# Kernel optimization log

Hardware: AMD Instinct MI355X
Metric: run time of the kernel (lower is better)

Reference implementation:

```python
import jax, jax.numpy as jnp
import numpy as np

N = 100000        # nodes
E = 1600000       # edges (avg degree 16)
IN = 128          # in_channels
HID = 256         # hidden_channels
OUT = 2           # out_channels
G = 512           # num graphs in batch


def setup_inputs() -> dict:
    key = jax.random.key(0)
    ks = jax.random.split(key, 10)
    x = jax.random.normal(ks[0], (N, IN), dtype=jnp.float32)
    edge_index = jax.random.randint(ks[1], (2, E), 0, N, dtype=jnp.int64)
    # sorted graph assignment, every graph non-empty (PyG-style batching)
    batch = (jnp.arange(N, dtype=jnp.int64) * G) // N
    s = 1.0 / np.sqrt(IN)
    sh = 1.0 / np.sqrt(2 * HID)
    sh1 = 1.0 / np.sqrt(HID)
    W_l = jax.random.uniform(ks[2], (HID, IN), jnp.float32, -s, s)   # SAGE lin_l (neighbors)
    b_l = jax.random.uniform(ks[3], (HID,), jnp.float32, -s, s)
    W_r = jax.random.uniform(ks[4], (HID, IN), jnp.float32, -s, s)   # SAGE lin_r (root), no bias
    W0 = jax.random.uniform(ks[5], (HID, IN), jnp.float32, -s, s)    # lin0
    b0 = jax.random.uniform(ks[5], (HID,), jnp.float32, -s, s)
    W1 = jax.random.uniform(ks[6], (HID, 2 * HID), jnp.float32, -sh, sh)  # lin1
    b1 = jax.random.uniform(ks[7], (HID,), jnp.float32, -sh, sh)
    W2 = jax.random.uniform(ks[8], (OUT, HID), jnp.float32, -sh1, sh1)    # lin2
    b2 = jax.random.uniform(ks[9], (OUT,), jnp.float32, -sh1, sh1)
    return {"x": x, "edge_index": edge_index, "batch": batch,
            "W_l": W_l, "b_l": b_l, "W_r": W_r,
            "W0": W0, "b0": b0, "W1": W1, "b1": b1, "W2": W2, "b2": b2}


def reference(x, edge_index, batch, W_l, b_l, W_r, W0, b0, W1, b1, W2, b2):
    src, dst = edge_index[0], edge_index[1]
    # SAGEConv: mean-aggregate neighbor features (gather -> scatter-add -> normalize)
    msg_sum = jax.ops.segment_sum(x[src], dst, num_segments=N)          # [N, IN]
    deg = jax.ops.segment_sum(jnp.ones((E,), x.dtype), dst, num_segments=N)
    aggr = msg_sum / jnp.maximum(deg, 1.0)[:, None]
    h = jax.nn.relu(aggr @ W_l.T + b_l + x @ W_r.T)                     # [N, HID]
    # global max pool per graph
    hp = jax.ops.segment_max(h, batch, num_segments=G)                  # [G, HID]
    # root node = first node of each graph (batch is sorted)
    root = jnp.searchsorted(batch, jnp.arange(G, dtype=batch.dtype))    # [G]
    news = jax.nn.relu(x[root] @ W0.T + b0)                             # [G, HID]
    h = jax.nn.relu(jnp.concatenate([news, hp], axis=-1) @ W1.T + b1)   # [G, HID]
    h = h @ W2.T + b2                                                   # [G, OUT]
    return jax.nn.log_softmax(h, axis=-1)
```

## Files before the change

### kernel.cpp

```cpp
#include <hip/hip_runtime.h>
#include <hip/hip_bf16.h>
#include <math.h>
#include <stdint.h>

#define IN_C 128
#define HID  256
#define OUT_C 2

#define BSHIFT 8
#define BNODES 256
#define EPB 4096
#define HISTB 784
#define PADB 768

typedef __attribute__((ext_vector_type(8))) short short8;
typedef __attribute__((ext_vector_type(4))) float f32x4;
typedef __attribute__((ext_vector_type(2))) float f32x2;

#if defined(__has_builtin)
#if __has_builtin(__builtin_amdgcn_cvt_pk_f32_fp8) && __has_builtin(__builtin_amdgcn_cvt_pk_fp8_f32)
#define HAVE_FP8_CVT 1
#endif
#endif

__device__ __forceinline__ ushort f2bf(float f) {
  uint32_t u = __float_as_uint(f);
  uint32_t r = u + 0x7FFF + ((u >> 16) & 1);
  return (ushort)(r >> 16);
}
__device__ __forceinline__ float bf2f(ushort b) {
  return __uint_as_float(((uint32_t)b) << 16);
}

#ifndef HAVE_FP8_CVT
__device__ __forceinline__ uint32_t f2fp8_1(float f) {
  uint32_t u = __float_as_uint(f);
  uint32_t s = (u >> 24) & 0x80;
  float a = fabsf(f);
  if (a >= 448.f) return s | 0x7E;
  if (a < 0.015625f) {
    uint32_t m = (uint32_t)(a * 512.f + 0.5f);
    return s | m;
  }
  uint32_t r = u & 0x7fffffff;
  r += 0x7FFFF + ((r >> 20) & 1);
  uint32_t e = (r >> 23) - 127;
  if ((int)e > 8) return s | 0x7E;
  return s | ((e + 7) << 3) | ((r >> 20) & 7);
}
__device__ __forceinline__ float fp8_2f(uint32_t b) {
  uint32_t s = (b & 0x80) << 24;
  uint32_t e = (b >> 3) & 0xF, m = b & 7;
  if (e == 0) { float f = (float)m * 0.001953125f; return s ? -f : f; }
  return __uint_as_float(s | ((e + 120) << 23) | (m << 20));
}
#endif

__device__ __forceinline__ void acc8f8v(f32x2* s, uint2 v) {
#ifdef HAVE_FP8_CVT
  s[0] += __builtin_amdgcn_cvt_pk_f32_fp8(v.x, false);
  s[1] += __builtin_amdgcn_cvt_pk_f32_fp8(v.x, true);
  s[2] += __builtin_amdgcn_cvt_pk_f32_fp8(v.y, false);
  s[3] += __builtin_amdgcn_cvt_pk_f32_fp8(v.y, true);
#else
  s[0].x += fp8_2f(v.x & 0xff);         s[0].y += fp8_2f((v.x >> 8) & 0xff);
  s[1].x += fp8_2f((v.x >> 16) & 0xff); s[1].y += fp8_2f(v.x >> 24);
  s[2].x += fp8_2f(v.y & 0xff);         s[2].y += fp8_2f((v.y >> 8) & 0xff);
  s[3].x += fp8_2f((v.y >> 16) & 0xff); s[3].y += fp8_2f(v.y >> 24);
#endif
}


__global__ void k_prep(const float* __restrict__ x, ushort* __restrict__ xb,
                       uint32_t* __restrict__ xf8, int n4,
                       const float* __restrict__ Wl, const float* __restrict__ Wr,
                       ushort* __restrict__ Wcat,
                       const float* __restrict__ W0, ushort* __restrict__ W0b,
                       const float* __restrict__ W1, ushort* __restrict__ W1b,
                       const int* __restrict__ batch, int* __restrict__ root, int n,
                       const int* __restrict__ dst, int E, int* __restrict__ bcount,
                       float* __restrict__ hp, int hp4) {
  __shared__ int h[512];
  int t = threadIdx.x;
  int i = blockIdx.x * 256 + t;
  if (i < n4) {
    float4 v = ((const float4*)x)[i];
    ushort4 o = {f2bf(v.x), f2bf(v.y), f2bf(v.z), f2bf(v.w)};
    ((ushort4*)xb)[i] = o;
#ifdef HAVE_FP8_CVT
    int p = __builtin_amdgcn_cvt_pk_fp8_f32(v.x, v.y, 0, false);
    p = __builtin_amdgcn_cvt_pk_fp8_f32(v.z, v.w, p, true);
    xf8[i] = (uint32_t)p;
#else
    xf8[i] = f2fp8_1(v.x) | (f2fp8_1(v.y) << 8) | (f2fp8_1(v.z) << 16) |
             (f2fp8_1(v.w) << 24);
#endif
  }
  if (i < 32) xf8[(size_t)n * 32 + i] = 0;
  if (i < HID * (2 * IN_C) / 4) {
    int c = i >> 6, c4 = (i & 63) * 4;
    float4 v = (c4 < IN_C) ? *(const float4*)(Wl + (size_t)c * IN_C + c4)
                           : *(const float4*)(Wr + (size_t)c * IN_C + (c4 - IN_C));
    ushort4 o = {f2bf(v.x), f2bf(v.y), f2bf(v.z), f2bf(v.w)};
    *(ushort4*)(Wcat + (size_t)c * (2 * IN_C) + c4) = o;
  }
  if (i < HID * IN_C / 4) {
    float4 v = ((const float4*)W0)[i];
    ushort4 o = {f2bf(v.x), f2bf(v.y), f2bf(v.z), f2bf(v.w)};
    ((ushort4*)W0b)[i] = o;
  }
  if (i < HID * 2 * HID / 4) {
    float4 v = ((const float4*)W1)[i];
    ushort4 o = {f2bf(v.x), f2bf(v.y), f2bf(v.z), f2bf(v.w)};
    ((ushort4*)W1b)[i] = o;
  }
  if (i < hp4) ((float4*)hp)[i] = make_float4(0.f, 0.f, 0.f, 0.f);
  if (i < n) {
    int g = batch[i];
    if (i == 0 || batch[i - 1] != g) root[g] = i;
  }
  if (blockIdx.x < HISTB) {
    h[t] = 0; h[t + 256] = 0;
    __syncthreads();
    int E4 = E >> 2;
    const int4* d4 = (const int4*)dst;
    for (int e = blockIdx.x * 256 + t; e < E4; e += HISTB * 256) {
      int4 d = d4[e];
      atomicAdd(&h[d.x >> BSHIFT], 1);
      atomicAdd(&h[d.y >> BSHIFT], 1);
      atomicAdd(&h[d.z >> BSHIFT], 1);
      atomicAdd(&h[d.w >> BSHIFT], 1);
    }
    if (blockIdx.x == 0)
      for (int e = (E4 << 2) + t; e < E; e += 256)
        atomicAdd(&h[dst[e] >> BSHIFT], 1);
    __syncthreads();
    if (h[t]) atomicAdd(&bcount[t], h[t]);
    if (h[t + 256]) atomicAdd(&bcount[t + 256], h[t + 256]);
  }
}


__global__ __launch_bounds__(256) void k_scatter(
    const int* __restrict__ src, const int* __restrict__ dst,
    const int* __restrict__ bcount, int* __restrict__ cursor0,
    uint32_t* __restrict__ rec, int E) {
  __shared__ int sBB[512];
  __shared__ int stmp[256];
  __shared__ int h[512];
  __shared__ int hb[512];
  __shared__ int lcur[512];
  int t = threadIdx.x;
  int c0 = bcount[2 * t], c1 = bcount[2 * t + 1];
  stmp[t] = c0 + c1;
  h[2 * t] = 0; h[2 * t + 1] = 0;
  lcur[2 * t] = 0; lcur[2 * t + 1] = 0;
  __syncthreads();
  for (int off = 1; off < 256; off <<= 1) {
    int v = (t >= off) ? stmp[t - off] : 0;
    __syncthreads();
    stmp[t] += v;
    __syncthreads();
  }
  int ex = stmp[t] - (c0 + c1);
  sBB[2 * t] = ex;
  sBB[2 * t + 1] = ex + c0;
  __syncthreads();

  int e0 = blockIdx.x * EPB;
  int e1 = e0 + EPB < E ? e0 + EPB : E;
  int cnt = e1 - e0;
  int cnt4 = cnt >> 2;
  const int4* d4 = (const int4*)(dst + e0);
  const int4* s4 = (const int4*)(src + e0);

  for (int i = t; i < cnt4; i += 256) {
    int4 d = d4[i];
    atomicAdd(&h[d.x >> BSHIFT], 1);
    atomicAdd(&h[d.y >> BSHIFT], 1);
    atomicAdd(&h[d.z >> BSHIFT], 1);
    atomicAdd(&h[d.w >> BSHIFT], 1);
  }
  for (int i = (cnt4 << 2) + t; i < cnt; i += 256)
    atomicAdd(&h[dst[e0 + i] >> BSHIFT], 1);
  __syncthreads();
  for (int j = t; j < 512; j += 256)
    if (h[j]) hb[j] = sBB[j] + atomicAdd(&cursor0[j], h[j]);
  __syncthreads();
  for (int i = t; i < cnt4; i += 256) {
    int4 d = d4[i];
    int4 s = s4[i];
    {
      int b = d.x >> BSHIFT; int r = atomicAdd(&lcur[b], 1);
      rec[hb[b] + r] = ((uint32_t)s.x << BSHIFT) | ((uint32_t)d.x & (BNODES - 1));
    }
    {
      int b = d.y >> BSHIFT; int r = atomicAdd(&lcur[b], 1);
      rec[hb[b] + r] = ((uint32_t)s.y << BSHIFT) | ((uint32_t)d.y & (BNODES - 1));
    }
    {
      int b = d.z >> BSHIFT; int r = atomicAdd(&lcur[b], 1);
      rec[hb[b] + r] = ((uint32_t)s.z << BSHIFT) | ((uint32_t)d.z & (BNODES - 1));
    }
    {
      int b = d.w >> BSHIFT; int r = atomicAdd(&lcur[b], 1);
      rec[hb[b] + r] = ((uint32_t)s.w << BSHIFT) | ((uint32_t)d.w & (BNODES - 1));
    }
  }
  for (int i = (cnt4 << 2) + t; i < cnt; i += 256) {
    int d = dst[e0 + i];
    int b = d >> BSHIFT;
    int r = atomicAdd(&lcur[b], 1);
    rec[hb[b] + r] = ((uint32_t)src[e0 + i] << BSHIFT) | ((uint32_t)d & (BNODES - 1));
  }
}


__global__ __launch_bounds__(256) void k_csr(
    const uint32_t* __restrict__ rec, const int* __restrict__ bcount,
    int* __restrict__ row_start, int* __restrict__ deg,
    int* __restrict__ csr, int n, int zrow) {
  __shared__ int stmp[256];
  __shared__ int lexcl[256];
  __shared__ int ldeg[256];
  __shared__ int lcur[256];
  int t = threadIdx.x, b = blockIdx.x;
  int i2 = 2 * t;
  int v = ((i2 < b) ? bcount[i2] : 0) + ((i2 + 1 < b) ? bcount[i2 + 1] : 0);
  stmp[t] = v;
  ldeg[t] = 0;
  __syncthreads();
  for (int off = 128; off > 0; off >>= 1) {
    if (t < off) stmp[t] += stmp[t + off];
    __syncthreads();
  }
  int ebase = stmp[0];
  int ecnt = bcount[b];
  int padbase = ((ebase + 3) & ~3) + PADB * b;
  int node0 = b << BSHIFT;
  __syncthreads();

  const uint32_t* rb = rec + ebase;
  int ec4 = ecnt >> 2;
  for (int i = t; i < ec4; i += 256) {
    uint4 r = *(const uint4*)(rb + i * 4);
    atomicAdd(&ldeg[r.x & (BNODES - 1)], 1);
    atomicAdd(&ldeg[r.y & (BNODES - 1)], 1);
    atomicAdd(&ldeg[r.z & (BNODES - 1)], 1);
    atomicAdd(&ldeg[r.w & (BNODES - 1)], 1);
  }
  for (int i = (ec4 << 2) + t; i < ecnt; i += 256)
    atomicAdd(&ldeg[rb[i] & (BNODES - 1)], 1);
  __syncthreads();
  int d = ldeg[t];
  int P = (d + 3) & ~3;
  stmp[t] = P;
  __syncthreads();
  for (int off = 1; off < 256; off <<= 1) {
    int vv = (t >= off) ? stmp[t - off] : 0;
    __syncthreads();
    stmp[t] += vv;
    __syncthreads();
  }
  int excl = stmp[t] - P;
  lexcl[t] = excl;
  int rs = padbase + excl;
  int node = node0 + t;
  if (node < n) { row_start[node] = rs; deg[node] = d; }
  lcur[t] = 0;
  __syncthreads();
  for (int i = t; i < ec4; i += 256) {
    uint4 r = *(const uint4*)(rb + i * 4);
    {
      int li = r.x & (BNODES - 1); int k = atomicAdd(&lcur[li], 1);
      csr[padbase + lexcl[li] + k] = (int)(r.x >> BSHIFT);
    }
    {
      int li = r.y & (BNODES - 1); int k = atomicAdd(&lcur[li], 1);
      csr[padbase + lexcl[li] + k] = (int)(r.y >> BSHIFT);
    }
    {
      int li = r.z & (BNODES - 1); int k = atomicAdd(&lcur[li], 1);
      csr[padbase + lexcl[li] + k] = (int)(r.z >> BSHIFT);
    }
    {
      int li = r.w & (BNODES - 1); int k = atomicAdd(&lcur[li], 1);
      csr[padbase + lexcl[li] + k] = (int)(r.w >> BSHIFT);
    }
  }
  for (int i = (ec4 << 2) + t; i < ecnt; i += 256) {
    uint32_t r = rb[i];
    int li = r & (BNODES - 1);
    int k = atomicAdd(&lcur[li], 1);
    csr[padbase + lexcl[li] + k] = (int)(r >> BSHIFT);
  }
  for (int k = d; k < P; ++k) csr[rs + k] = zrow;
}


__global__ void k_aggr(const uint32_t* __restrict__ xf8, const int* __restrict__ csr,
                       const int* __restrict__ row_start, const int* __restrict__ deg,
                       ushort* __restrict__ aggr, int n) {
  int wid = threadIdx.x >> 6;
  int lane = threadIdx.x & 63;
  int q = lane >> 4, li = lane & 15;
  int node = blockIdx.x * 16 + wid * 4 + q;
  bool alive = node < n;
  int base = alive ? row_start[node] : 0;
  int d = alive ? deg[node] : 0;
  int P = (d + 3) & ~3;
  const uint2* xp = (const uint2*)xf8 + li;
  f32x2 s[4] = {};
  for (int i = 0; i < P; i += 4) {
    int4 ns = *(const int4*)(csr + base + i);
    uint2 a = xp[(size_t)ns.x * 16];
    uint2 b = xp[(size_t)ns.y * 16];
    uint2 c = xp[(size_t)ns.z * 16];
    uint2 e = xp[(size_t)ns.w * 16];
    acc8f8v(s, a); acc8f8v(s, b); acc8f8v(s, c); acc8f8v(s, e);
  }
  if (alive) {
    float inv = 1.0f / (float)(d > 1 ? d : 1);
    uint4 o;
    o.x = (uint32_t)f2bf(s[0].x * inv) | ((uint32_t)f2bf(s[0].y * inv) << 16);
    o.y = (uint32_t)f2bf(s[1].x * inv) | ((uint32_t)f2bf(s[1].y * inv) << 16);
    o.z = (uint32_t)f2bf(s[2].x * inv) | ((uint32_t)f2bf(s[2].y * inv) << 16);
    o.w = (uint32_t)f2bf(s[3].x * inv) | ((uint32_t)f2bf(s[3].y * inv) << 16);
    ((uint4*)(aggr + (size_t)node * IN_C))[li] = o;
  }
}


__global__ __launch_bounds__(256) void k_gemm_pool(
    const ushort* __restrict__ aggrb, const ushort* __restrict__ xb,
    const ushort* __restrict__ Wcat, const float* __restrict__ bl,
    const int* __restrict__ batch, float* __restrict__ hp, int n) {
  __shared__ float sbl[256];
  __shared__ int sBatch[64];

  int t = threadIdx.x;
  int n0 = blockIdx.x * 64;
  sbl[t] = bl[t];
  if (t < 64) sBatch[t] = (n0 + t < n) ? batch[n0 + t] : -1;
  __syncthreads();

  int lane = t & 63, w = t >> 6;
  int q = lane >> 4, m = lane & 15;

  const ushort* arow[4];
  const ushort* xrow[4];
  const ushort* wrow[4];
#pragma unroll
  for (int rt = 0; rt < 4; ++rt) {
    int gn = n0 + rt * 16 + m; gn = gn < n ? gn : n - 1;
    arow[rt] = aggrb + (size_t)gn * IN_C + q * 8;
    xrow[rt] = xb + (size_t)gn * IN_C + q * 8;
  }
#pragma unroll
  for (int ct = 0; ct < 4; ++ct)
    wrow[ct] = Wcat + (size_t)(w * 64 + ct * 16 + m) * (2 * IN_C) + q * 8;

  short8 afn[4], bfn[4];
#pragma unroll
  for (int rt = 0; rt < 4; ++rt) afn[rt] = *(const short8*)arow[rt];
#pragma unroll
  for (int ct = 0; ct < 4; ++ct) bfn[ct] = *(const short8*)wrow[ct];

  f32x4 acc[4][4] = {};
#pragma unroll
  for (int kc = 0; kc < 8; ++kc) {
    short8 af[4], bf[4];
#pragma unroll
    for (int rt = 0; rt < 4; ++rt) af[rt] = afn[rt];
#pragma unroll
    for (int ct = 0; ct < 4; ++ct) bf[ct] = bfn[ct];
    if (kc < 7) {
      int kn = kc + 1;
#pragma unroll
      for (int rt = 0; rt < 4; ++rt)
        afn[rt] = (kn < 4) ? *(const short8*)(arow[rt] + kn * 32)
                           : *(const short8*)(xrow[rt] + (kn - 4) * 32);
#pragma unroll
      for (int ct = 0; ct < 4; ++ct)
        bfn[ct] = *(const short8*)(wrow[ct] + kn * 32);
    }
#pragma unroll
    for (int rt = 0; rt < 4; ++rt)
#pragma unroll
      for (int ct = 0; ct < 4; ++ct)
        acc[rt][ct] = __builtin_amdgcn_mfma_f32_16x16x32_bf16(af[rt], bf[ct], acc[rt][ct], 0, 0, 0);
  }

  int last = n - 1 - n0; last = last < 63 ? last : 63;
  int gA = sBatch[0];
  int gB = sBatch[last];
#pragma unroll
  for (int ct = 0; ct < 4; ++ct) {
    int col = w * 64 + ct * 16 + m;
    float bias = sbl[col];
    float mA = 0.f, mB = 0.f;
#pragma unroll
    for (int rt = 0; rt < 4; ++rt) {
#pragma unroll
      for (int i = 0; i < 4; ++i) {
        int lr = rt * 16 + q * 4 + i;
        if (n0 + lr < n) {
          float v = fmaxf(acc[rt][ct][i] + bias, 0.f);
          if (sBatch[lr] == gA) mA = fmaxf(mA, v);
          else mB = fmaxf(mB, v);
        }
      }
    }
    mA = fmaxf(mA, __shfl_xor(mA, 16)); mA = fmaxf(mA, __shfl_xor(mA, 32));
    mB = fmaxf(mB, __shfl_xor(mB, 16)); mB = fmaxf(mB, __shfl_xor(mB, 32));
    if (q == 0) {
      atomicMax((int*)&hp[(size_t)gA * HID + col], __float_as_int(mA));
      if (gB != gA) atomicMax((int*)&hp[(size_t)gB * HID + col], __float_as_int(mB));
    }
  }
}


__global__ __launch_bounds__(256) void k_tail(
    const ushort* __restrict__ xb, const float* __restrict__ hp,
    const int* __restrict__ root,
    const ushort* __restrict__ W0b, const float* __restrict__ b0,
    const ushort* __restrict__ W1b, const float* __restrict__ b1,
    const float* __restrict__ W2, const float* __restrict__ b2,
    float* __restrict__ out, int G) {
  __shared__ ushort sCat[32][264];
  __shared__ int sRoot[32];
  __shared__ float pp[256][2];

  int t = threadIdx.x;
  int g0 = blockIdx.x * 32;
  if (t < 32) sRoot[t] = (g0 + t < G) ? root[g0 + t] : 0;
  __syncthreads();

  int lane = t & 63, w = t >> 6;
  int q = lane >> 4, m = lane & 15;

  const ushort* xrow[2];
#pragma unroll
  for (int rt = 0; rt < 2; ++rt)
    xrow[rt] = xb + (size_t)sRoot[rt * 16 + m] * IN_C;

  {
    f32x4 acc[2][4] = {};
#pragma unroll
    for (int kc = 0; kc < 4; ++kc) {
      short8 af[2], bf[4];
#pragma unroll
      for (int rt = 0; rt < 2; ++rt)
        af[rt] = *(const short8*)(xrow[rt] + kc * 32 + q * 8);
#pragma unroll
      for (int ct = 0; ct < 4; ++ct) {
        int col = w * 64 + ct * 16 + m;
        bf[ct] = *(const short8*)(W0b + (size_t)col * IN_C + kc * 32 + q * 8);
      }
#pragma unroll
      for (int rt = 0; rt < 2; ++rt)
#pragma unroll
        for (int ct = 0; ct < 4; ++ct)
          acc[rt][ct] = __builtin_amdgcn_mfma_f32_16x16x32_bf16(af[rt], bf[ct], acc[rt][ct], 0, 0, 0);
    }
#pragma unroll
    for (int ct = 0; ct < 4; ++ct) {
      int col = w * 64 + ct * 16 + m;
      float bias = b0[col];
#pragma unroll
      for (int rt = 0; rt < 2; ++rt)
#pragma unroll
        for (int i = 0; i < 4; ++i) {
          int row = rt * 16 + q * 4 + i;
          sCat[row][col] = f2bf(fmaxf(acc[rt][ct][i] + bias, 0.f));
        }
    }
  }
  __syncthreads();

  f32x4 acc2[2][4] = {};
  short8 bfn[4];
#pragma unroll
  for (int ct = 0; ct < 4; ++ct)
    bfn[ct] = *(const short8*)(W1b + (size_t)(w * 64 + ct * 16 + m) * (2 * HID) + q * 8);
#pragma unroll
  for (int kc = 0; kc < 8; ++kc) {
    short8 af[2], bf[4];
#pragma unroll
    for (int ct = 0; ct < 4; ++ct) bf[ct] = bfn[ct];
    if (kc < 7) {
#pragma unroll
      for (int ct = 0; ct < 4; ++ct)
        bfn[ct] = *(const short8*)(W1b + (size_t)(w * 64 + ct * 16 + m) * (2 * HID) +
                                   (kc + 1) * 32 + q * 8);
    }
#pragma unroll
    for (int rt = 0; rt < 2; ++rt)
      af[rt] = *(const short8*)&sCat[rt * 16 + m][kc * 32 + q * 8];
#pragma unroll
    for (int rt = 0; rt < 2; ++rt)
#pragma unroll
      for (int ct = 0; ct < 4; ++ct)
        acc2[rt][ct] = __builtin_amdgcn_mfma_f32_16x16x32_bf16(af[rt], bf[ct], acc2[rt][ct], 0, 0, 0);
  }
  __syncthreads();
#pragma unroll
  for (int it = 0; it < 8; ++it) {
    int idx = it * 256 + t;
    int r = idx >> 6, c4 = (idx & 63) * 4;
    if (g0 + r < G) {
      float4 v = *(const float4*)(hp + (size_t)(g0 + r) * HID + c4);
      ushort4 o = {f2bf(v.x), f2bf(v.y), f2bf(v.z), f2bf(v.w)};
      *(ushort4*)&sCat[r][c4] = o;
    }
  }
  __syncthreads();
#pragma unroll
  for (int ct = 0; ct < 4; ++ct)
    bfn[ct] = *(const short8*)(W1b + (size_t)(w * 64 + ct * 16 + m) * (2 * HID) + 8 * 32 + q * 8);
#pragma unroll
  for (int kc = 8; kc < 16; ++kc) {
    short8 af[2], bf[4];
#pragma unroll
    for (int ct = 0; ct < 4; ++ct) bf[ct] = bfn[ct];
    if (kc < 15) {
#pragma unroll
      for (int ct = 0; ct < 4; ++ct)
        bfn[ct] = *(const short8*)(W1b + (size_t)(w * 64 + ct * 16 + m) * (2 * HID) +
                                   (kc + 1) * 32 + q * 8);
    }
#pragma unroll
    for (int rt = 0; rt < 2; ++rt)
      af[rt] = *(const short8*)&sCat[rt * 16 + m][(kc - 8) * 32 + q * 8];
#pragma unroll
    for (int rt = 0; rt < 2; ++rt)
#pragma unroll
      for (int ct = 0; ct < 4; ++ct)
        acc2[rt][ct] = __builtin_amdgcn_mfma_f32_16x16x32_bf16(af[rt], bf[ct], acc2[rt][ct], 0, 0, 0);
  }
  __syncthreads();
#pragma unroll
  for (int ct = 0; ct < 4; ++ct) {
    int col = w * 64 + ct * 16 + m;
    float bias = b1[col];
#pragma unroll
    for (int rt = 0; rt < 2; ++rt)
#pragma unroll
      for (int i = 0; i < 4; ++i) {
        int row = rt * 16 + q * 4 + i;
        sCat[row][col] = f2bf(fmaxf(acc2[rt][ct][i] + bias, 0.f));
      }
  }
  __syncthreads();

  {
    int row = t >> 3, qq = t & 7;
    float p0 = 0.f, p1 = 0.f;
    for (int c = qq * 32; c < qq * 32 + 32; ++c) {
      float hv = bf2f(sCat[row][c]);
      p0 += hv * W2[c];
      p1 += hv * W2[HID + c];
    }
    pp[t][0] = p0; pp[t][1] = p1;
  }
  __syncthreads();
  if (t < 32 && g0 + t < G) {
    float l0 = b2[0], l1 = b2[1];
#pragma unroll
    for (int k = 0; k < 8; ++k) { l0 += pp[t * 8 + k][0]; l1 += pp[t * 8 + k][1]; }
    float mx = fmaxf(l0, l1);
    float ls = logf(expf(l0 - mx) + expf(l1 - mx));
    out[(size_t)(g0 + t) * 2 + 0] = l0 - mx - ls;
    out[(size_t)(g0 + t) * 2 + 1] = l1 - mx - ls;
  }
}


extern "C" void kernel_launch(void* const* d_in, const int* in_sizes, int n_in,
                              void* d_out, int out_size, void* d_ws, size_t ws_size,
                              hipStream_t stream) {
  const float* x  = (const float*)d_in[0];
  const int* ei   = (const int*)d_in[1];
  const int* batch= (const int*)d_in[2];
  const float* Wl = (const float*)d_in[3];
  const float* bl = (const float*)d_in[4];
  const float* Wr = (const float*)d_in[5];
  const float* W0 = (const float*)d_in[6];
  const float* b0 = (const float*)d_in[7];
  const float* W1 = (const float*)d_in[8];
  const float* b1 = (const float*)d_in[9];
  const float* W2 = (const float*)d_in[10];
  const float* b2 = (const float*)d_in[11];
  float* out = (float*)d_out;

  const int N = in_sizes[0] / IN_C;
  const int E = in_sizes[1] / 2;
  const int G = out_size / OUT_C;
  const int* src = ei;
  const int* dst = ei + E;
  const int NB = (N + BNODES - 1) >> BSHIFT;

  char* w = (char*)d_ws;
  int* deg       = (int*)w; w += (size_t)N * 4;
  int* row_start = (int*)w; w += (size_t)N * 4;
  int* bcount    = (int*)w; w += 2048;
  int* cursor0   = (int*)w; w += 2048;
  int* root      = (int*)w; w += (size_t)G * 4;
  w = (char*)(((uintptr_t)w + 255) & ~(uintptr_t)255);
  int* csr       = (int*)w; w += (size_t)(E + PADB * NB + 8192) * 4;
  w = (char*)(((uintptr_t)w + 255) & ~(uintptr_t)255);
  ushort* xb     = (ushort*)w; w += (size_t)N * IN_C * 2;
  uint32_t* xf8  = (uint32_t*)w; w += (size_t)(N + 1) * IN_C;
  ushort* aggrb  = (ushort*)w; w += (size_t)N * IN_C * 2;
  ushort* Wcat   = (ushort*)w; w += (size_t)HID * (2 * IN_C) * 2;
  ushort* W0b    = (ushort*)w; w += (size_t)HID * IN_C * 2;
  ushort* W1b    = (ushort*)w; w += (size_t)HID * 2 * HID * 2;
  float* hp      = (float*)w; w += (size_t)G * HID * 4;
  uint32_t* rec  = (uint32_t*)aggrb;

  hipMemsetAsync(bcount, 0, 4096, stream);

  int n4 = N * IN_C / 4;
  k_prep<<<(n4 + 255) / 256, 256, 0, stream>>>(
      x, xb, xf8, n4, Wl, Wr, Wcat, W0, W0b, W1, W1b, batch, root, N,
      dst, E, bcount, hp, G * HID / 4);
  k_scatter<<<(E + EPB - 1) / EPB, 256, 0, stream>>>(src, dst, bcount, cursor0, rec, E);
  k_csr<<<NB, 256, 0, stream>>>(rec, bcount, row_start, deg, csr, N, N);
  k_aggr<<<(N + 15) / 16, 256, 0, stream>>>(xf8, csr, row_start, deg, aggrb, N);
  k_gemm_pool<<<(N + 63) / 64, 256, 0, stream>>>(aggrb, xb, Wcat, bl, batch, hp, N);
  k_tail<<<(G + 31) / 32, 256, 0, stream>>>(xb, hp, root, W0b, b0, W1b, b1, W2, b2, out, G);
}
```

Before: 283.7 us.

## Fuse neighbor aggregation into GEMM+pool kernel via swizzled LDS tiles

New measurement: 275.4 us. 2.9% less time.

```diff
diff --git a/kernel.cpp b/kernel.cpp
--- a/kernel.cpp
+++ b/kernel.cpp
@@ -20,6 +20,9 @@
 #if defined(__has_builtin)
 #if __has_builtin(__builtin_amdgcn_cvt_pk_f32_fp8) && __has_builtin(__builtin_amdgcn_cvt_pk_fp8_f32)
 #define HAVE_FP8_CVT 1
+#endif
+#if __has_builtin(__builtin_amdgcn_global_load_lds)
+#define HAVE_GLL 1
 #endif
 #endif
 
@@ -298,91 +301,103 @@
 }
 
 
-__global__ void k_aggr(const uint32_t* __restrict__ xf8, const int* __restrict__ csr,
-                       const int* __restrict__ row_start, const int* __restrict__ deg,
-                       ushort* __restrict__ aggr, int n) {
-  int wid = threadIdx.x >> 6;
-  int lane = threadIdx.x & 63;
-  int q = lane >> 4, li = lane & 15;
-  int node = blockIdx.x * 16 + wid * 4 + q;
-  bool alive = node < n;
-  int base = alive ? row_start[node] : 0;
-  int d = alive ? deg[node] : 0;
-  int P = (d + 3) & ~3;
+#ifdef HAVE_GLL
+__device__ __forceinline__ void load16_lds(const ushort* g, ushort* l) {
+  __builtin_amdgcn_global_load_lds(
+      (const __attribute__((address_space(1))) uint32_t*)g,
+      (__attribute__((address_space(3))) uint32_t*)l, 16, 0, 0);
+}
+#endif
+
+__global__ __launch_bounds__(256) void k_fused(
+    const uint32_t* __restrict__ xf8, const ushort* __restrict__ xb,
+    const int* __restrict__ csr, const int* __restrict__ row_start,
+    const int* __restrict__ deg,
+    const ushort* __restrict__ Wcat, const float* __restrict__ bl,
+    const int* __restrict__ batch, float* __restrict__ hp, int n) {
+  __shared__ ushort sAg[64 * 128];
+  __shared__ ushort sX[64 * 128];
+  __shared__ float sbl[256];
+  __shared__ int sBatch[64];
+
+  int t = threadIdx.x;
+  int n0 = blockIdx.x * 64;
+  sbl[t] = bl[t];
+  if (t < 64) sBatch[t] = (n0 + t < n) ? batch[n0 + t] : -1;
+
+  int lane = t & 63, w = t >> 6;
+  int q = lane >> 4, m = lane & 15;
+  int li = m;
+
+#pragma unroll
+  for (int j = 0; j < 4; ++j) {
+    int s = (j * 4 + w) * 64 + lane;
+    int r = s >> 4, p16 = s & 15;
+    int c16 = p16 ^ (r & 15);
+    int gn = n0 + r; gn = gn < n ? gn : n - 1;
+    const ushort* g = xb + (size_t)gn * IN_C + c16 * 8;
+#ifdef HAVE_GLL
+    load16_lds(g, &sX[(size_t)s * 8]);
+#else
+    *(uint4*)&sX[(size_t)s * 8] = *(const uint4*)g;
+#endif
+  }
+
   const uint2* xp = (const uint2*)xf8 + li;
-  f32x2 s[4] = {};
-  for (int i = 0; i < P; i += 4) {
-    int4 ns = *(const int4*)(csr + base + i);
-    uint2 a = xp[(size_t)ns.x * 16];
-    uint2 b = xp[(size_t)ns.y * 16];
-    uint2 c = xp[(size_t)ns.z * 16];
-    uint2 e = xp[(size_t)ns.w * 16];
-    acc8f8v(s, a); acc8f8v(s, b); acc8f8v(s, c); acc8f8v(s, e);
-  }
-  if (alive) {
+#pragma unroll
+  for (int pass = 0; pass < 4; ++pass) {
+    int r = pass * 16 + w * 4 + q;
+    int node = n0 + r;
+    bool alive = node < n;
+    int base = alive ? row_start[node] : 0;
+    int d = alive ? deg[node] : 0;
+    int P = (d + 3) & ~3;
+    f32x2 s[4] = {};
+    for (int i = 0; i < P; i += 4) {
+      int4 ns = *(const int4*)(csr + base + i);
+      uint2 a = xp[(size_t)ns.x * 16];
+      uint2 b = xp[(size_t)ns.y * 16];
+      uint2 c = xp[(size_t)ns.z * 16];
+      uint2 e = xp[(size_t)ns.w * 16];
+      acc8f8v(s, a); acc8f8v(s, b); acc8f8v(s, c); acc8f8v(s, e);
+    }
     float inv = 1.0f / (float)(d > 1 ? d : 1);
     uint4 o;
     o.x = (uint32_t)f2bf(s[0].x * inv) | ((uint32_t)f2bf(s[0].y * inv) << 16);
     o.y = (uint32_t)f2bf(s[1].x * inv) | ((uint32_t)f2bf(s[1].y * inv) << 16);
     o.z = (uint32_t)f2bf(s[2].x * inv) | ((uint32_t)f2bf(s[2].y * inv) << 16);
     o.w = (uint32_t)f2bf(s[3].x * inv) | ((uint32_t)f2bf(s[3].y * inv) << 16);
-    ((uint4*)(aggr + (size_t)node * IN_C))[li] = o;
-  }
-}
-
-
-__global__ __launch_bounds__(256) void k_gemm_pool(
-    const ushort* __restrict__ aggrb, const ushort* __restrict__ xb,
-    const ushort* __restrict__ Wcat, const float* __restrict__ bl,
-    const int* __restrict__ batch, float* __restrict__ hp, int n) {
-  __shared__ float sbl[256];
-  __shared__ int sBatch[64];
-
-  int t = threadIdx.x;
-  int n0 = blockIdx.x * 64;
-  sbl[t] = bl[t];
-  if (t < 64) sBatch[t] = (n0 + t < n) ? batch[n0 + t] : -1;
-  __syncthreads();
-
-  int lane = t & 63, w = t >> 6;
-  int q = lane >> 4, m = lane & 15;
-
-  const ushort* arow[4];
-  const ushort* xrow[4];
-  const ushort* wrow[4];
-#pragma unroll
-  for (int rt = 0; rt < 4; ++rt) {
-    int gn = n0 + rt * 16 + m; gn = gn < n ? gn : n - 1;
-    arow[rt] = aggrb + (size_t)gn * IN_C + q * 8;
-    xrow[rt] = xb + (size_t)gn * IN_C + q * 8;
-  }
+    int p = li ^ (r & 15);
+    *(uint4*)&sAg[r * 128 + p * 8] = o;
+  }
+
+  short8 bf_n[4];
 #pragma unroll
   for (int ct = 0; ct < 4; ++ct)
-    wrow[ct] = Wcat + (size_t)(w * 64 + ct * 16 + m) * (2 * IN_C) + q * 8;
-
-  short8 afn[4], bfn[4];
-#pragma unroll
-  for (int rt = 0; rt < 4; ++rt) afn[rt] = *(const short8*)arow[rt];
-#pragma unroll
-  for (int ct = 0; ct < 4; ++ct) bfn[ct] = *(const short8*)wrow[ct];
+    bf_n[ct] = *(const short8*)(Wcat + (size_t)(w * 64 + ct * 16 + m) * (2 * IN_C) + q * 8);
+
+  __syncthreads();
 
   f32x4 acc[4][4] = {};
 #pragma unroll
   for (int kc = 0; kc < 8; ++kc) {
-    short8 af[4], bf[4];
-#pragma unroll
-    for (int rt = 0; rt < 4; ++rt) af[rt] = afn[rt];
-#pragma unroll
-    for (int ct = 0; ct < 4; ++ct) bf[ct] = bfn[ct];
+    short8 bf[4];
+#pragma unroll
+    for (int ct = 0; ct < 4; ++ct) bf[ct] = bf_n[ct];
     if (kc < 7) {
-      int kn = kc + 1;
-#pragma unroll
-      for (int rt = 0; rt < 4; ++rt)
-        afn[rt] = (kn < 4) ? *(const short8*)(arow[rt] + kn * 32)
-                           : *(const short8*)(xrow[rt] + (kn - 4) * 32);
 #pragma unroll
       for (int ct = 0; ct < 4; ++ct)
-        bfn[ct] = *(const short8*)(wrow[ct] + kn * 32);
+        bf_n[ct] = *(const short8*)(Wcat + (size_t)(w * 64 + ct * 16 + m) * (2 * IN_C) +
+                                    (kc + 1) * 32 + q * 8);
+    }
+    const ushort* half = (kc < 4) ? sAg : sX;
+    int lc = ((kc & 3) * 4 + q);
+    short8 af[4];
+#pragma unroll
+    for (int rt = 0; rt < 4; ++rt) {
+      int r = rt * 16 + m;
+      int p = lc ^ m;
+      af[rt] = *(const short8*)&half[r * 128 + p * 8];
     }
 #pragma unroll
     for (int rt = 0; rt < 4; ++rt)
@@ -610,14 +625,14 @@
   w = (char*)(((uintptr_t)w + 255) & ~(uintptr_t)255);
   int* csr       = (int*)w; w += (size_t)(E + PADB * NB + 8192) * 4;
   w = (char*)(((uintptr_t)w + 255) & ~(uintptr_t)255);
+  uint32_t* rec  = (uint32_t*)w; w += (size_t)E * 4;
+  w = (char*)(((uintptr_t)w + 255) & ~(uintptr_t)255);
   ushort* xb     = (ushort*)w; w += (size_t)N * IN_C * 2;
   uint32_t* xf8  = (uint32_t*)w; w += (size_t)(N + 1) * IN_C;
-  ushort* aggrb  = (ushort*)w; w += (size_t)N * IN_C * 2;
   ushort* Wcat   = (ushort*)w; w += (size_t)HID * (2 * IN_C) * 2;
   ushort* W0b    = (ushort*)w; w += (size_t)HID * IN_C * 2;
   ushort* W1b    = (ushort*)w; w += (size_t)HID * 2 * HID * 2;
   float* hp      = (float*)w; w += (size_t)G * HID * 4;
-  uint32_t* rec  = (uint32_t*)aggrb;
 
   hipMemsetAsync(bcount, 0, 4096, stream);
 
@@ -627,7 +642,7 @@
       dst, E, bcount, hp, G * HID / 4);
   k_scatter<<<(E + EPB - 1) / EPB, 256, 0, stream>>>(src, dst, bcount, cursor0, rec, E);
   k_csr<<<NB, 256, 0, stream>>>(rec, bcount, row_start, deg, csr, N, N);
-  k_aggr<<<(N + 15) / 16, 256, 0, stream>>>(xf8, csr, row_start, deg, aggrb, N);
-  k_gemm_pool<<<(N + 63) / 64, 256, 0, stream>>>(aggrb, xb, Wcat, bl, batch, hp, N);
+  k_fused<<<(N + 63) / 64, 256, 0, stream>>>(xf8, xb, csr, row_start, deg,
+                                             Wcat, bl, batch, hp, N);
   k_tail<<<(G + 31) / 32, 256, 0, stream>>>(xb, hp, root, W0b, b0, W1b, b1, W2, b2, out, G);
 }
```
